# Kernel optimization log

Measured on AMD Instinct MI355X. Metric: run time of the kernel, lower is better.

Reference implementation:

```python
import jax, jax.numpy as jnp
import numpy as np

N = 100000
E = 1600000
D = 128          # f_gru_in == f_gru_out
G = 128          # f_gather
K = 4            # n_etypes
STEPS = 3        # n_gconv_steps


def setup_inputs() -> dict:
    key = jax.random.key(0)
    ks = jax.random.split(key, 16)
    s = 0.05
    return {
        "features": jax.random.normal(ks[0], (N, D), jnp.float32),
        "src": jax.random.randint(ks[1], (E,), 0, N, jnp.int32),
        "dst": jax.random.randint(ks[2], (E,), 0, N, jnp.int32),
        "etypes": jax.random.randint(ks[3], (E,), 0, K, jnp.int32),
        # per-etype edge linears (torch Linear: y = x W^T + b)
        "W_et": jax.random.normal(ks[4], (K, D, D), jnp.float32) * s,
        "b_et": jax.random.normal(ks[5], (K, D), jnp.float32) * s,
        # GRUCell weights, torch gate order (r, z, n)
        "W_ih": jax.random.normal(ks[6], (3 * D, D), jnp.float32) * s,
        "b_ih": jax.random.normal(ks[7], (3 * D,), jnp.float32) * s,
        "W_hh": jax.random.normal(ks[8], (3 * D, D), jnp.float32) * s,
        "b_hh": jax.random.normal(ks[9], (3 * D,), jnp.float32) * s,
        # gated output head
        "i_w": jax.random.normal(ks[10], (G, D + D), jnp.float32) * s,
        "i_b": jax.random.normal(ks[11], (G,), jnp.float32) * s,
        "j_w": jax.random.normal(ks[12], (G, D), jnp.float32) * s,
        "j_b": jax.random.normal(ks[13], (G,), jnp.float32) * s,
    }


def _gru_cell(a, h, W_ih, b_ih, W_hh, b_hh):
    gi = a @ W_ih.T + b_ih          # [N, 3D]
    gh = h @ W_hh.T + b_hh          # [N, 3D]
    ir, iz, in_ = jnp.split(gi, 3, axis=1)
    hr, hz, hn = jnp.split(gh, 3, axis=1)
    r = jax.nn.sigmoid(ir + hr)
    z = jax.nn.sigmoid(iz + hz)
    n = jnp.tanh(in_ + r * hn)
    return (1.0 - z) * n + z * h


def reference(features, src, dst, etypes, W_et, b_et, W_ih, b_ih, W_hh, b_hh,
              i_w, i_b, j_w, j_b):
    n_nodes = features.shape[0]
    h = features  # in_feats == out_feats -> no zero padding needed
    for _ in range(STEPS):
        # transform all nodes by every etype linear: [K, N, D]
        t = jnp.einsum('nd,kod->kno', h, W_et) + b_et[:, None, :]
        # gather per-edge message by (etype, src) then scatter-add to dst
        msg = t[etypes, src]                                  # [E, D]
        a = jax.ops.segment_sum(msg, dst, num_segments=n_nodes)
        h = _gru_cell(a, h, W_ih, b_ih, W_hh, b_hh)
    # dropout p=0 (eval) -> identity; gated output head
    gate = jax.nn.sigmoid(jnp.concatenate([h, features], axis=1) @ i_w.T + i_b)
    return gate * (h @ j_w.T + j_b)
```

## Files before the change

### kernel.cpp

```cpp
#include <hip/hip_runtime.h>
#include <hip/hip_bf16.h>

typedef __bf16 bf16;
typedef __attribute__((ext_vector_type(8))) __bf16 bf16x8;
typedef __attribute__((ext_vector_type(4))) float f32x4;

union BP { unsigned u; bf16 b[2]; };

struct Desc {
  const void* A1; const bf16* W1; int lda1;
  const void* A2; const bf16* W2; int lda2;
  const bf16* b1; const bf16* b2;
  int coff; int a2mode;
};
struct Desc4 { Desc d[4]; };

template<int NK>
__global__ __launch_bounds__(256) void gemm_k(Desc4 P, bf16* __restrict__ C, int ldc,
                                              int M, const int* __restrict__ flagp)
{
  const Desc d = P.d[blockIdx.y];
  const int lane = threadIdx.x & 63;
  const int w    = threadIdx.x >> 6;
  const int quad = lane >> 4;
  const int lr   = lane & 15;
  const int mbase = blockIdx.x * 128 + w * 32;

  __shared__ bf16 lds[128 * 136];

  f32x4 acc[2][8];
#pragma unroll
  for (int i = 0; i < 2; ++i)
#pragma unroll
    for (int j = 0; j < 8; ++j) acc[i][j] = (f32x4){0.f, 0.f, 0.f, 0.f};

  long r0 = mbase + lr;      if (r0 >= M) r0 = M - 1;
  long r1 = mbase + 16 + lr; if (r1 >= M) r1 = M - 1;

  {
    const bf16* A = (const bf16*)d.A1;
    const int lda = d.lda1;
#pragma unroll
    for (int kk = 0; kk < NK; ++kk) {
      const int kc = kk * 32 + quad * 8;
      bf16x8 a0 = *(const bf16x8*)(A + r0 * lda + kc);
      bf16x8 a1 = *(const bf16x8*)(A + r1 * lda + kc);
#pragma unroll
      for (int ct = 0; ct < 8; ++ct) {
        bf16x8 b = *(const bf16x8*)(d.W1 + ((size_t)(kk * 8 + ct) * 64 + lane) * 8);
        acc[0][ct] = __builtin_amdgcn_mfma_f32_16x16x32_bf16(a0, b, acc[0][ct], 0, 0, 0);
        acc[1][ct] = __builtin_amdgcn_mfma_f32_16x16x32_bf16(a1, b, acc[1][ct], 0, 0, 0);
      }
    }
  }
  if (d.a2mode != 0) {
    const int lda = d.lda2;
    const bool f32 = (d.a2mode == 2) && (*flagp != 0);
    if (f32) {
      const float* A = (const float*)d.A2;
#pragma unroll
      for (int kk = 0; kk < NK; ++kk) {
        const int kc = kk * 32 + quad * 8;
        f32x4 x0 = *(const f32x4*)(A + r0 * lda + kc);
        f32x4 x1 = *(const f32x4*)(A + r0 * lda + kc + 4);
        f32x4 y0 = *(const f32x4*)(A + r1 * lda + kc);
        f32x4 y1 = *(const f32x4*)(A + r1 * lda + kc + 4);
        bf16x8 a0, a1;
#pragma unroll
        for (int i = 0; i < 4; ++i) {
          a0[i] = (bf16)x0[i]; a0[i + 4] = (bf16)x1[i];
          a1[i] = (bf16)y0[i]; a1[i + 4] = (bf16)y1[i];
        }
#pragma unroll
        for (int ct = 0; ct < 8; ++ct) {
          bf16x8 b = *(const bf16x8*)(d.W2 + ((size_t)(kk * 8 + ct) * 64 + lane) * 8);
          acc[0][ct] = __builtin_amdgcn_mfma_f32_16x16x32_bf16(a0, b, acc[0][ct], 0, 0, 0);
          acc[1][ct] = __builtin_amdgcn_mfma_f32_16x16x32_bf16(a1, b, acc[1][ct], 0, 0, 0);
        }
      }
    } else {
      const bf16* A = (const bf16*)d.A2;
#pragma unroll
      for (int kk = 0; kk < NK; ++kk) {
        const int kc = kk * 32 + quad * 8;
        bf16x8 a0 = *(const bf16x8*)(A + r0 * lda + kc);
        bf16x8 a1 = *(const bf16x8*)(A + r1 * lda + kc);
#pragma unroll
        for (int ct = 0; ct < 8; ++ct) {
          bf16x8 b = *(const bf16x8*)(d.W2 + ((size_t)(kk * 8 + ct) * 64 + lane) * 8);
          acc[0][ct] = __builtin_amdgcn_mfma_f32_16x16x32_bf16(a0, b, acc[0][ct], 0, 0, 0);
          acc[1][ct] = __builtin_amdgcn_mfma_f32_16x16x32_bf16(a1, b, acc[1][ct], 0, 0, 0);
        }
      }
    }
  }

#pragma unroll
  for (int ct = 0; ct < 8; ++ct) {
    const int nl = ct * 16 + lr;
    float bv = 0.f;
    if (d.b1) bv += (float)d.b1[nl];
    if (d.b2) bv += (float)d.b2[nl];
#pragma unroll
    for (int rt = 0; rt < 2; ++rt) {
      const int rowb = w * 32 + rt * 16 + quad * 4;
#pragma unroll
      for (int r = 0; r < 4; ++r)
        lds[(rowb + r) * 136 + nl] = (bf16)(acc[rt][ct][r] + bv);
    }
  }
  __syncthreads();
  const int tr = threadIdx.x >> 4;
  const int tc = (threadIdx.x & 15) * 8;
#pragma unroll
  for (int i = 0; i < 8; ++i) {
    const int row = i * 16 + tr;
    const int grow = blockIdx.x * 128 + row;
    if (grow < M) {
      bf16x8 v = *(const bf16x8*)(lds + row * 136 + tc);
      *(bf16x8*)(C + (size_t)grow * ldc + d.coff + tc) = v;
    }
  }
}

__global__ __launch_bounds__(256) void fused_k(const bf16* __restrict__ big,
                                               bf16* __restrict__ hbp,
                                               const bf16* __restrict__ wb,
                                               int M)
{
  const int lane = threadIdx.x & 63;
  const int w    = threadIdx.x >> 6;
  const int quad = lane >> 4;
  const int lr   = lane & 15;
  const int mbase = blockIdx.x * 128 + w * 32;

  __shared__ bf16 lds[128 * 136];

  const bf16* wcat = wb;
  const bf16* blk  = wb + 69632;
  const bf16 *ih0 = blk,             *ih1 = blk + 16384, *ihn = blk + 2 * 16384;
  const bf16 *hh0 = blk + 3 * 16384, *hh1 = blk + 4 * 16384, *hhn = blk + 5 * 16384;
  const bf16 *bih = wb + 217088, *bhh = wb + 217472;

  long r0 = mbase + lr;      if (r0 >= M) r0 = M - 1;
  long r1 = mbase + 16 + lr; if (r1 >= M) r1 = M - 1;

  f32x4 acc[2][8];
#pragma unroll
  for (int i = 0; i < 2; ++i)
#pragma unroll
    for (int j = 0; j < 8; ++j) acc[i][j] = (f32x4){0.f, 0.f, 0.f, 0.f};

  bf16x8 Bb[2][8];
  bf16x8 Ab[4][2];
#pragma unroll
  for (int q = 0; q < 4; ++q) {
    const int kc = q * 32 + quad * 8;
    Ab[q][0] = *(const bf16x8*)(big + r0 * 544 + kc);
    Ab[q][1] = *(const bf16x8*)(big + r1 * 544 + kc);
  }
#pragma unroll
  for (int q = 0; q < 2; ++q) {
#pragma unroll
    for (int ct = 0; ct < 8; ++ct)
      Bb[q][ct] = *(const bf16x8*)(wcat + ((size_t)(q * 8 + ct) * 64 + lane) * 8);
  }
#pragma unroll
  for (int kk = 0; kk < 17; ++kk) {
    const int pa = kk & 3;
    const int pb = kk & 1;
#pragma unroll
    for (int ct = 0; ct < 8; ++ct) {
      acc[0][ct] = __builtin_amdgcn_mfma_f32_16x16x32_bf16(Ab[pa][0], Bb[pb][ct], acc[0][ct], 0, 0, 0);
      acc[1][ct] = __builtin_amdgcn_mfma_f32_16x16x32_bf16(Ab[pa][1], Bb[pb][ct], acc[1][ct], 0, 0, 0);
    }
    if (kk + 4 < 17) {
      const int k4 = kk + 4;
      const int kc = k4 * 32 + quad * 8;
      Ab[pa][0] = *(const bf16x8*)(big + r0 * 544 + kc);
      Ab[pa][1] = *(const bf16x8*)(big + r1 * 544 + kc);
    }
    if (kk + 2 < 17) {
      const int k2 = kk + 2;
#pragma unroll
      for (int ct = 0; ct < 8; ++ct)
        Bb[pb][ct] = *(const bf16x8*)(wcat + ((size_t)(k2 * 8 + ct) * 64 + lane) * 8);
    }
  }

  bf16x8 hf[2][4];
#pragma unroll
  for (int kk = 0; kk < 4; ++kk) {
    hf[0][kk] = *(const bf16x8*)(hbp + r0 * 128 + kk * 32 + quad * 8);
    hf[1][kk] = *(const bf16x8*)(hbp + r1 * 128 + kk * 32 + quad * 8);
  }

#pragma unroll
  for (int ct = 0; ct < 8; ++ct) {
    const int nl = ct * 16 + lr;
#pragma unroll
    for (int rt = 0; rt < 2; ++rt) {
      const int rowb = w * 32 + rt * 16 + quad * 4;
#pragma unroll
      for (int r = 0; r < 4; ++r)
        lds[(rowb + r) * 136 + nl] = (bf16)acc[rt][ct][r];
    }
  }
  bf16x8 af[2][4];
#pragma unroll
  for (int kk = 0; kk < 4; ++kk) {
    af[0][kk] = *(const bf16x8*)(lds + (w * 32 + lr) * 136 + kk * 32 + quad * 8);
    af[1][kk] = *(const bf16x8*)(lds + (w * 32 + 16 + lr) * 136 + kk * 32 + quad * 8);
  }
#pragma unroll
  for (int kk = 0; kk < 4; ++kk) {
    *(bf16x8*)(lds + (w * 32 + lr) * 136 + kk * 32 + quad * 8)      = hf[0][kk];
    *(bf16x8*)(lds + (w * 32 + 16 + lr) * 136 + kk * 32 + quad * 8) = hf[1][kk];
  }

  bf16x8 Gb[2][6];
#pragma unroll
  for (int q = 0; q < 2; ++q) {
    const size_t wi = ((size_t)(q * 8 + 0) * 64 + lane) * 8;
    Gb[q][0] = *(const bf16x8*)(ih0 + wi);
    Gb[q][1] = *(const bf16x8*)(hh0 + wi);
    Gb[q][2] = *(const bf16x8*)(ih1 + wi);
    Gb[q][3] = *(const bf16x8*)(hh1 + wi);
    Gb[q][4] = *(const bf16x8*)(ihn + wi);
    Gb[q][5] = *(const bf16x8*)(hhn + wi);
  }

#pragma unroll
  for (int ch = 0; ch < 8; ++ch) {
    f32x4 c[4][2];
#pragma unroll
    for (int s = 0; s < 4; ++s)
#pragma unroll
      for (int i = 0; i < 2; ++i) c[s][i] = (f32x4){0.f, 0.f, 0.f, 0.f};

#pragma unroll
    for (int kk = 0; kk < 4; ++kk) {
      const int G = ch * 4 + kk;
      const int p = G & 1;
      c[0][0] = __builtin_amdgcn_mfma_f32_16x16x32_bf16(af[0][kk], Gb[p][0], c[0][0], 0, 0, 0);
      c[0][1] = __builtin_amdgcn_mfma_f32_16x16x32_bf16(af[1][kk], Gb[p][0], c[0][1], 0, 0, 0);
      c[0][0] = __builtin_amdgcn_mfma_f32_16x16x32_bf16(hf[0][kk], Gb[p][1], c[0][0], 0, 0, 0);
      c[0][1] = __builtin_amdgcn_mfma_f32_16x16x32_bf16(hf[1][kk], Gb[p][1], c[0][1], 0, 0, 0);
      c[1][0] = __builtin_amdgcn_mfma_f32_16x16x32_bf16(af[0][kk], Gb[p][2], c[1][0], 0, 0, 0);
      c[1][1] = __builtin_amdgcn_mfma_f32_16x16x32_bf16(af[1][kk], Gb[p][2], c[1][1], 0, 0, 0);
      c[1][0] = __builtin_amdgcn_mfma_f32_16x16x32_bf16(hf[0][kk], Gb[p][3], c[1][0], 0, 0, 0);
      c[1][1] = __builtin_amdgcn_mfma_f32_16x16x32_bf16(hf[1][kk], Gb[p][3], c[1][1], 0, 0, 0);
      c[2][0] = __builtin_amdgcn_mfma_f32_16x16x32_bf16(af[0][kk], Gb[p][4], c[2][0], 0, 0, 0);
      c[2][1] = __builtin_amdgcn_mfma_f32_16x16x32_bf16(af[1][kk], Gb[p][4], c[2][1], 0, 0, 0);
      c[3][0] = __builtin_amdgcn_mfma_f32_16x16x32_bf16(hf[0][kk], Gb[p][5], c[3][0], 0, 0, 0);
      c[3][1] = __builtin_amdgcn_mfma_f32_16x16x32_bf16(hf[1][kk], Gb[p][5], c[3][1], 0, 0, 0);
      if (G + 2 < 32) {
        const int G2 = G + 2;
        const int ch2 = G2 >> 2, kk2 = G2 & 3;
        const int ct2 = ch2;
        const size_t wi2 = ((size_t)(kk2 * 8 + ct2) * 64 + lane) * 8;
        Gb[p][0] = *(const bf16x8*)(ih0 + wi2);
        Gb[p][1] = *(const bf16x8*)(hh0 + wi2);
        Gb[p][2] = *(const bf16x8*)(ih1 + wi2);
        Gb[p][3] = *(const bf16x8*)(hh1 + wi2);
        Gb[p][4] = *(const bf16x8*)(ihn + wi2);
        Gb[p][5] = *(const bf16x8*)(hhn + wi2);
      }
    }
    {
      const int col = ch * 16 + lr;
      const float br = (float)bih[col]       + (float)bhh[col];
      const float bz = (float)bih[128 + col] + (float)bhh[128 + col];
      const float bi = (float)bih[256 + col];
      const float bh = (float)bhh[256 + col];
#pragma unroll
      for (int rt = 0; rt < 2; ++rt) {
        const int rowb = w * 32 + rt * 16 + quad * 4;
#pragma unroll
        for (int r = 0; r < 4; ++r) {
          const int li = (rowb + r) * 136 + col;
          const float hv = (float)lds[li];
          const float rr = 1.f / (1.f + __expf(-(c[0][rt][r] + br)));
          const float zz = 1.f / (1.f + __expf(-(c[1][rt][r] + bz)));
          const float xn = c[2][rt][r] + bi + rr * (c[3][rt][r] + bh);
          const float e2 = __expf(2.f * xn);
          const float nn = 1.f - 2.f / (e2 + 1.f);
          lds[li] = (bf16)((1.f - zz) * nn + zz * hv);
        }
      }
    }
  }

  __syncthreads();
  const int tr = threadIdx.x >> 4;
  const int tc = (threadIdx.x & 15) * 8;
#pragma unroll
  for (int i = 0; i < 8; ++i) {
    const int row = i * 16 + tr;
    const int grow = blockIdx.x * 128 + row;
    if (grow < M) {
      bf16x8 v = *(const bf16x8*)(lds + row * 136 + tc);
      *(bf16x8*)(hbp + (size_t)grow * 128 + tc) = v;
    }
  }
}

__global__ __launch_bounds__(256) void detect_k(const unsigned short* __restrict__ f,
                                                int n16, int* __restrict__ flag)
{
  int i = blockIdx.x * 256 + threadIdx.x;
  int bad = 0;
  for (int j = i; j < n16; j += 256 * 1024) {
    int ex = (f[j] >> 7) & 0xFF;
    if (ex >= 0x87) bad = 1;
  }
  if (bad) atomicAdd(flag, 1);
}

__global__ __launch_bounds__(256) void feat_k(const void* __restrict__ src,
                                              bf16* __restrict__ hb, int n,
                                              const int* __restrict__ flag)
{
  int i = blockIdx.x * 256 + threadIdx.x;
  if (i >= n) return;
  if (*flag) hb[i] = (bf16)((const float*)src)[i];
  else       hb[i] = ((const bf16*)src)[i];
}

__global__ __launch_bounds__(256) void cvtw_k(
    const void* w_et, const void* b_et, const void* w_ih, const void* b_ih,
    const void* w_hh, const void* b_hh, const void* i_w, const void* i_b,
    const void* j_w, const void* j_b, bf16* __restrict__ wb,
    const int* __restrict__ flagp)
{
  int i = blockIdx.x * 256 + threadIdx.x;
  if (i >= 218112) return;
  const bool f32 = (*flagp != 0);
  auto rd = [&](const void* p, int idx) -> float {
    return f32 ? ((const float*)p)[idx] : (float)((const bf16*)p)[idx];
  };
  float v;
  if (i < 69632) {
    int e = i, j = e & 7, lane = (e >> 3) & 63, ct = (e >> 9) & 7, kk = e >> 12;
    int n = ct * 16 + (lane & 15), k = kk * 32 + (lane >> 4) * 8 + j;
    if (k < 512)      v = rd(w_et, (k >> 7) * 16384 + n * 128 + (k & 127));
    else if (k < 516) v = rd(b_et, (k - 512) * 128 + n);
    else              v = 0.f;
  } else if (i < 217088) {
    int blk = (i - 69632) >> 14, e = (i - 69632) & 16383;
    int j = e & 7, lane = (e >> 3) & 63, ct = (e >> 9) & 7, kk = e >> 12;
    int n = ct * 16 + (lane & 15), k = kk * 32 + (lane >> 4) * 8 + j;
    const void* src; int idx;
    switch (blk) {
      case 0: src = w_ih; idx = n * 128 + k; break;
      case 1: src = w_ih; idx = (128 + n) * 128 + k; break;
      case 2: src = w_ih; idx = (256 + n) * 128 + k; break;
      case 3: src = w_hh; idx = n * 128 + k; break;
      case 4: src = w_hh; idx = (128 + n) * 128 + k; break;
      case 5: src = w_hh; idx = (256 + n) * 128 + k; break;
      case 6: src = i_w;  idx = n * 256 + k; break;
      case 7: src = i_w;  idx = n * 256 + 128 + k; break;
      default: src = j_w; idx = n * 128 + k; break;
    }
    v = rd(src, idx);
  } else {
    int o = i - 217088;
    if (o < 384)      v = rd(b_ih, o);
    else if (o < 768) v = rd(b_hh, o - 384);
    else if (o < 896) v = rd(i_b, o - 768);
    else              v = rd(j_b, o - 896);
  }
  wb[i] = (bf16)v;
}

__global__ __launch_bounds__(256) void hist_k(const int* __restrict__ dst,
                                              const int* __restrict__ ety,
                                              int* __restrict__ deg, int E)
{
  int e = blockIdx.x * 256 + threadIdx.x;
  if (e < E) atomicAdd(&deg[dst[e] * 4 + ety[e]], 1);
}

__global__ __launch_bounds__(512) void scan1_k(const int* __restrict__ deg, int* __restrict__ rp,
                                               int* __restrict__ part, int n)
{
  __shared__ int buf[512];
  int i = blockIdx.x * 512 + threadIdx.x;
  int v = (i < n) ? deg[i] : 0;
  buf[threadIdx.x] = v;
  __syncthreads();
#pragma unroll
  for (int off = 1; off < 512; off <<= 1) {
    int t = 0;
    if (threadIdx.x >= off) t = buf[threadIdx.x - off];
    __syncthreads();
    buf[threadIdx.x] += t;
    __syncthreads();
  }
  if (i < n) rp[i] = buf[threadIdx.x] - v;
  if (threadIdx.x == 511) part[blockIdx.x] = buf[511];
}

__global__ __launch_bounds__(1024) void scan2_k(int* __restrict__ part, int nb, int* __restrict__ total)
{
  __shared__ int buf[1024];
  int t0 = threadIdx.x;
  int v = (t0 < nb) ? part[t0] : 0;
  buf[t0] = v;
  __syncthreads();
#pragma unroll
  for (int off = 1; off < 1024; off <<= 1) {
    int t = 0;
    if (t0 >= off) t = buf[t0 - off];
    __syncthreads();
    buf[t0] += t;
    __syncthreads();
  }
  if (t0 < nb) part[t0] = buf[t0] - v;
  if (t0 == 1023) *total = buf[1023];
}

__global__ __launch_bounds__(512) void scan3_k(int* __restrict__ rp, const int* __restrict__ part, int n)
{
  int i = blockIdx.x * 512 + threadIdx.x;
  if (i < n) rp[i] += part[blockIdx.x];
}

__global__ __launch_bounds__(256) void fill_k(const int* __restrict__ src, const int* __restrict__ dst,
                                              const int* __restrict__ ety, const int* __restrict__ rp,
                                              int* __restrict__ fil, int* __restrict__ bkt, int E)
{
  int e = blockIdx.x * 256 + threadIdx.x;
  if (e < E) {
    int key = dst[e] * 4 + ety[e];
    int pos = rp[key] + atomicAdd(&fil[key], 1);
    bkt[pos] = src[e];
  }
}

__global__ __launch_bounds__(256) void agg_k(const bf16* __restrict__ hb,
                                             const int* __restrict__ rp,
                                             const int* __restrict__ bkt,
                                             bf16* __restrict__ aggH, int N)
{
  const int lane = threadIdx.x & 63;
  const int n = blockIdx.x * 4 + (threadIdx.x >> 6);
  if (n >= N) return;
  const unsigned* hp = (const unsigned*)hb;
  unsigned* outp = (unsigned*)aggH + (size_t)n * 272;
  const int e0 = rp[n * 4];
  const int e1 = rp[n * 4 + 1];
  const int e2 = rp[n * 4 + 2];
  const int e3 = rp[n * 4 + 3];
  const int e4 = rp[n * 4 + 4];
  const int last = e4 - 1;
  float a00 = 0.f, a01 = 0.f, a10 = 0.f, a11 = 0.f;
  float a20 = 0.f, a21 = 0.f, a30 = 0.f, a31 = 0.f;
  for (int base = e0; base < e4; base += 8) {
    int b[8];
#pragma unroll
    for (int t = 0; t < 8; ++t) {
      const int i = base + t;
      b[t] = bkt[i <= last ? i : last];
    }
    unsigned u[8];
#pragma unroll
    for (int t = 0; t < 8; ++t)
      u[t] = hp[(size_t)b[t] * 64 + lane];
#pragma unroll
    for (int t = 0; t < 8; ++t) {
      const int i = base + t;
      BP tt; tt.u = u[t];
      const bool ok = (i <= last);
      const float v0 = ok ? (float)tt.b[0] : 0.f;
      const float v1 = ok ? (float)tt.b[1] : 0.f;
      const bool s0 = i < e1;
      const bool s1 = (i >= e1) && (i < e2);
      const bool s2 = (i >= e2) && (i < e3);
      const bool s3 = (i >= e3);
      a00 += s0 ? v0 : 0.f;  a01 += s0 ? v1 : 0.f;
      a10 += s1 ? v0 : 0.f;  a11 += s1 ? v1 : 0.f;
      a20 += s2 ? v0 : 0.f;  a21 += s2 ? v1 : 0.f;
      a30 += s3 ? v0 : 0.f;  a31 += s3 ? v1 : 0.f;
    }
  }
  BP o;
  o.b[0] = (bf16)a00; o.b[1] = (bf16)a01; outp[0 * 64 + lane] = o.u;
  o.b[0] = (bf16)a10; o.b[1] = (bf16)a11; outp[1 * 64 + lane] = o.u;
  o.b[0] = (bf16)a20; o.b[1] = (bf16)a21; outp[2 * 64 + lane] = o.u;
  o.b[0] = (bf16)a30; o.b[1] = (bf16)a31; outp[3 * 64 + lane] = o.u;
  if (lane < 16) {
    BP z; z.b[0] = (bf16)0.f; z.b[1] = (bf16)0.f;
    if (lane == 0) { z.b[0] = (bf16)(float)(e1 - e0); z.b[1] = (bf16)(float)(e2 - e1); }
    if (lane == 1) { z.b[0] = (bf16)(float)(e3 - e2); z.b[1] = (bf16)(float)(e4 - e3); }
    outp[256 + lane] = z.u;
  }
}

__global__ __launch_bounds__(256) void head_k(const bf16* __restrict__ G,
                                              void* __restrict__ out, int N,
                                              const int* __restrict__ flag)
{
  int i = blockIdx.x * 256 + threadIdx.x;
  if (i >= N * 64) return;
  int n = i >> 6, l = i & 63;
  const unsigned* g = (const unsigned*)G + (size_t)n * 128;
  BP gl, uu;
  gl.u = g[l]; uu.u = g[64 + l];
  float v0 = (float)uu.b[0] / (1.f + expf(-(float)gl.b[0]));
  float v1 = (float)uu.b[1] / (1.f + expf(-(float)gl.b[1]));
  if (*flag) {
    ((float*)out)[(size_t)n * 128 + 2 * l]     = v0;
    ((float*)out)[(size_t)n * 128 + 2 * l + 1] = v1;
  } else {
    BP o; o.b[0] = (bf16)v0; o.b[1] = (bf16)v1;
    ((unsigned*)out)[(size_t)n * 64 + l] = o.u;
  }
}

extern "C" void kernel_launch(void* const* d_in, const int* in_sizes, int n_in,
                              void* d_out, int out_size, void* d_ws, size_t ws_size,
                              hipStream_t stream)
{
  const void* feat = d_in[0];
  const int*  src  = (const int*)d_in[1];
  const int*  dst  = (const int*)d_in[2];
  const int*  ety  = (const int*)d_in[3];

  const int N = in_sizes[0] / 128;
  const int E = in_sizes[1];
  const int total = N * 128;

  char* p = (char*)d_ws;
  auto alloc = [&](size_t bytes) -> char* {
    char* q = p;
    p += (bytes + 255) & ~(size_t)255;
    return q;
  };
  bf16* big  = (bf16*)alloc((size_t)N * 544 * 2);
  bf16* hb   = (bf16*)alloc((size_t)total * 2);
  bf16* wb   = (bf16*)alloc(218112 * 2);
  int*  rp   = (int*) alloc(((size_t)4 * N + 1) * 4);
  int*  deg  = (int*) alloc((size_t)4 * N * 4);
  int*  bkt  = (int*) alloc((size_t)E * 4);
  int*  part = (int*) alloc(1024 * 4);
  int*  flag = (int*) alloc(64);

  const int oBlk = 69632;
  const bf16 *iwa = wb + oBlk + 6 * 16384, *iwb = wb + oBlk + 7 * 16384,
             *jw  = wb + oBlk + 8 * 16384;
  const bf16 *ib = wb + 217856, *jb = wb + 217984;

  const int gE  = (E + 255) / 256;
  const int gT  = (total + 255) / 256;
  const int gM  = (N + 127) / 128;
  const int n4  = 4 * N;
  const int gS  = (n4 + 511) / 512;
  const int gH  = (N * 64 + 255) / 256;

  hipMemsetAsync(flag, 0, 4, stream);
  detect_k<<<1024, 256, 0, stream>>>((const unsigned short*)feat, 2000000, flag);
  feat_k<<<gT, 256, 0, stream>>>(feat, hb, total, flag);
  cvtw_k<<<(218112 + 255) / 256, 256, 0, stream>>>(
      d_in[4], d_in[5], d_in[6], d_in[7], d_in[8],
      d_in[9], d_in[10], d_in[11], d_in[12], d_in[13], wb, flag);

  hipMemsetAsync(deg, 0, (size_t)n4 * 4, stream);
  hist_k<<<gE, 256, 0, stream>>>(dst, ety, deg, E);
  scan1_k<<<gS, 512, 0, stream>>>(deg, rp, part, n4);
  scan2_k<<<1, 1024, 0, stream>>>(part, gS, rp + n4);
  scan3_k<<<gS, 512, 0, stream>>>(rp, part, n4);
  hipMemsetAsync(deg, 0, (size_t)n4 * 4, stream);
  fill_k<<<gE, 256, 0, stream>>>(src, dst, ety, rp, deg, bkt, E);

  Desc4 Ph = {};
  Ph.d[0] = { hb, iwa, 128, feat, iwb, 128, ib, nullptr, 0,   2 };
  Ph.d[1] = { hb, jw,  128, nullptr, nullptr, 0, jb, nullptr, 128, 0 };

  for (int step = 0; step < 3; ++step) {
    agg_k<<<(N + 3) / 4, 256, 0, stream>>>(hb, rp, bkt, big, N);
    fused_k<<<gM, 256, 0, stream>>>(big, hb, wb, N);
  }

  gemm_k<4><<<dim3(gM, 2), 256, 0, stream>>>(Ph, big, 256, N, flag);
  head_k<<<gH, 256, 0, stream>>>(big, d_out, N, flag);
}
```

Measured before the change: 996.1 us.

## Stage fused-kernel weight tiles through LDS via async global_load_lds double buffering

In the fused GRU kernel, each wave used to load weight fragments straight from global memory into registers, so all four waves fetched the same weights. Now each block loads every weight tile into a double-buffered LDS region once, using global_load_lds DMA, and waves read their fragments from LDS. The aim is to cut redundant global/L2 traffic and register pressure, which could allow more waves per CU. In exchange it adds a __syncthreads per k-step (17 in the first GEMM, 32 in the gate loop), turns the outer gate loop into a non-unrolled loop, and adds 16KB of LDS per block, which may lower occupancy.

```diff
diff --git a/kernel.cpp b/kernel.cpp
--- a/kernel.cpp
+++ b/kernel.cpp
@@ -6,6 +6,12 @@
 typedef __attribute__((ext_vector_type(4))) float f32x4;
 
 union BP { unsigned u; bf16 b[2]; };
+
+__device__ __forceinline__ void dma16(const void* g, void* l) {
+  __builtin_amdgcn_global_load_lds(
+      (const __attribute__((address_space(1))) unsigned*)g,
+      (__attribute__((address_space(3))) unsigned*)l, 16, 0, 0);
+}
 
 struct Desc {
   const void* A1; const bf16* W1; int lda1;
@@ -26,7 +32,7 @@
   const int lr   = lane & 15;
   const int mbase = blockIdx.x * 128 + w * 32;
 
-  __shared__ bf16 lds[128 * 136];
+  __shared__ __align__(16) bf16 lds[128 * 136];
 
   f32x4 acc[2][8];
 #pragma unroll
@@ -134,7 +140,8 @@
   const int lr   = lane & 15;
   const int mbase = blockIdx.x * 128 + w * 32;
 
-  __shared__ bf16 lds[128 * 136];
+  __shared__ __align__(16) bf16 lds[128 * 136];
+  __shared__ __align__(16) bf16 wlds[2][4096];
 
   const bf16* wcat = wb;
   const bf16* blk  = wb + 69632;
@@ -145,47 +152,50 @@
   long r0 = mbase + lr;      if (r0 >= M) r0 = M - 1;
   long r1 = mbase + 16 + lr; if (r1 >= M) r1 = M - 1;
 
+  dma16(wcat + (size_t)(w * 2)     * 512 + (size_t)lane * 8, &wlds[0][(w * 2) * 512]);
+  dma16(wcat + (size_t)(w * 2 + 1) * 512 + (size_t)lane * 8, &wlds[0][(w * 2 + 1) * 512]);
+  bf16x8 Ab[2][2];
+  Ab[0][0] = *(const bf16x8*)(big + r0 * 544 + quad * 8);
+  Ab[0][1] = *(const bf16x8*)(big + r1 * 544 + quad * 8);
+
   f32x4 acc[2][8];
 #pragma unroll
   for (int i = 0; i < 2; ++i)
 #pragma unroll
     for (int j = 0; j < 8; ++j) acc[i][j] = (f32x4){0.f, 0.f, 0.f, 0.f};
 
-  bf16x8 Bb[2][8];
-  bf16x8 Ab[4][2];
-#pragma unroll
-  for (int q = 0; q < 4; ++q) {
-    const int kc = q * 32 + quad * 8;
-    Ab[q][0] = *(const bf16x8*)(big + r0 * 544 + kc);
-    Ab[q][1] = *(const bf16x8*)(big + r1 * 544 + kc);
-  }
-#pragma unroll
-  for (int q = 0; q < 2; ++q) {
-#pragma unroll
-    for (int ct = 0; ct < 8; ++ct)
-      Bb[q][ct] = *(const bf16x8*)(wcat + ((size_t)(q * 8 + ct) * 64 + lane) * 8);
-  }
+  __syncthreads();
+
 #pragma unroll
   for (int kk = 0; kk < 17; ++kk) {
-    const int pa = kk & 3;
-    const int pb = kk & 1;
+    const int cur = kk & 1;
+    const int nxt = cur ^ 1;
+    if (kk + 1 < 17) {
+      const size_t gb = (size_t)(kk + 1) * 4096;
+      dma16(wcat + gb + (size_t)(w * 2)     * 512 + (size_t)lane * 8, &wlds[nxt][(w * 2) * 512]);
+      dma16(wcat + gb + (size_t)(w * 2 + 1) * 512 + (size_t)lane * 8, &wlds[nxt][(w * 2 + 1) * 512]);
+      const int kc = (kk + 1) * 32 + quad * 8;
+      Ab[nxt][0] = *(const bf16x8*)(big + r0 * 544 + kc);
+      Ab[nxt][1] = *(const bf16x8*)(big + r1 * 544 + kc);
+    }
 #pragma unroll
     for (int ct = 0; ct < 8; ++ct) {
-      acc[0][ct] = __builtin_amdgcn_mfma_f32_16x16x32_bf16(Ab[pa][0], Bb[pb][ct], acc[0][ct], 0, 0, 0);
-      acc[1][ct] = __builtin_amdgcn_mfma_f32_16x16x32_bf16(Ab[pa][1], Bb[pb][ct], acc[1][ct], 0, 0, 0);
-    }
-    if (kk + 4 < 17) {
-      const int k4 = kk + 4;
-      const int kc = k4 * 32 + quad * 8;
-      Ab[pa][0] = *(const bf16x8*)(big + r0 * 544 + kc);
-      Ab[pa][1] = *(const bf16x8*)(big + r1 * 544 + kc);
-    }
-    if (kk + 2 < 17) {
-      const int k2 = kk + 2;
-#pragma unroll
-      for (int ct = 0; ct < 8; ++ct)
-        Bb[pb][ct] = *(const bf16x8*)(wcat + ((size_t)(k2 * 8 + ct) * 64 + lane) * 8);
-    }
+      bf16x8 b = *(const bf16x8*)&wlds[cur][(ct * 64 + lane) * 8];
+      acc[0][ct] = __builtin_amdgcn_mfma_f32_16x16x32_bf16(Ab[cur][0], b, acc[0][ct], 0, 0, 0);
+      acc[1][ct] = __builtin_amdgcn_mfma_f32_16x16x32_bf16(Ab[cur][1], b, acc[1][ct], 0, 0, 0);
+    }
+    __syncthreads();
+  }
+
+  const bf16* wptr0 = ih0; const bf16* wptr1 = hh0; const bf16* wptr2 = ih1;
+  const bf16* wptr3 = hh1; const bf16* wptr4 = ihn; const bf16* wptr5 = hhn;
+  {
+    if (w == 0) { dma16(wptr0 + (size_t)lane * 8, &wlds[0][0 * 512]);
+                  dma16(wptr4 + (size_t)lane * 8, &wlds[0][4 * 512]); }
+    if (w == 1) { dma16(wptr1 + (size_t)lane * 8, &wlds[0][1 * 512]);
+                  dma16(wptr5 + (size_t)lane * 8, &wlds[0][5 * 512]); }
+    if (w == 2) { dma16(wptr2 + (size_t)lane * 8, &wlds[0][2 * 512]); }
+    if (w == 3) { dma16(wptr3 + (size_t)lane * 8, &wlds[0][3 * 512]); }
   }
 
   bf16x8 hf[2][4];
@@ -194,7 +204,6 @@
     hf[0][kk] = *(const bf16x8*)(hbp + r0 * 128 + kk * 32 + quad * 8);
     hf[1][kk] = *(const bf16x8*)(hbp + r1 * 128 + kk * 32 + quad * 8);
   }
-
 #pragma unroll
   for (int ct = 0; ct < 8; ++ct) {
     const int nl = ct * 16 + lr;
@@ -217,20 +226,9 @@
     *(bf16x8*)(lds + (w * 32 + lr) * 136 + kk * 32 + quad * 8)      = hf[0][kk];
     *(bf16x8*)(lds + (w * 32 + 16 + lr) * 136 + kk * 32 + quad * 8) = hf[1][kk];
   }
-
-  bf16x8 Gb[2][6];
-#pragma unroll
-  for (int q = 0; q < 2; ++q) {
-    const size_t wi = ((size_t)(q * 8 + 0) * 64 + lane) * 8;
-    Gb[q][0] = *(const bf16x8*)(ih0 + wi);
-    Gb[q][1] = *(const bf16x8*)(hh0 + wi);
-    Gb[q][2] = *(const bf16x8*)(ih1 + wi);
-    Gb[q][3] = *(const bf16x8*)(hh1 + wi);
-    Gb[q][4] = *(const bf16x8*)(ihn + wi);
-    Gb[q][5] = *(const bf16x8*)(hhn + wi);
-  }
-
-#pragma unroll
+  __syncthreads();
+
+#pragma unroll 1
   for (int ch = 0; ch < 8; ++ch) {
     f32x4 c[4][2];
 #pragma unroll
@@ -240,58 +238,64 @@
 
 #pragma unroll
     for (int kk = 0; kk < 4; ++kk) {
-      const int G = ch * 4 + kk;
-      const int p = G & 1;
-      c[0][0] = __builtin_amdgcn_mfma_f32_16x16x32_bf16(af[0][kk], Gb[p][0], c[0][0], 0, 0, 0);
-      c[0][1] = __builtin_amdgcn_mfma_f32_16x16x32_bf16(af[1][kk], Gb[p][0], c[0][1], 0, 0, 0);
-      c[0][0] = __builtin_amdgcn_mfma_f32_16x16x32_bf16(hf[0][kk], Gb[p][1], c[0][0], 0, 0, 0);
-      c[0][1] = __builtin_amdgcn_mfma_f32_16x16x32_bf16(hf[1][kk], Gb[p][1], c[0][1], 0, 0, 0);
-      c[1][0] = __builtin_amdgcn_mfma_f32_16x16x32_bf16(af[0][kk], Gb[p][2], c[1][0], 0, 0, 0);
-      c[1][1] = __builtin_amdgcn_mfma_f32_16x16x32_bf16(af[1][kk], Gb[p][2], c[1][1], 0, 0, 0);
-      c[1][0] = __builtin_amdgcn_mfma_f32_16x16x32_bf16(hf[0][kk], Gb[p][3], c[1][0], 0, 0, 0);
-      c[1][1] = __builtin_amdgcn_mfma_f32_16x16x32_bf16(hf[1][kk], Gb[p][3], c[1][1], 0, 0, 0);
-      c[2][0] = __builtin_amdgcn_mfma_f32_16x16x32_bf16(af[0][kk], Gb[p][4], c[2][0], 0, 0, 0);
-      c[2][1] = __builtin_amdgcn_mfma_f32_16x16x32_bf16(af[1][kk], Gb[p][4], c[2][1], 0, 0, 0);
-      c[3][0] = __builtin_amdgcn_mfma_f32_16x16x32_bf16(hf[0][kk], Gb[p][5], c[3][0], 0, 0, 0);
-      c[3][1] = __builtin_amdgcn_mfma_f32_16x16x32_bf16(hf[1][kk], Gb[p][5], c[3][1], 0, 0, 0);
-      if (G + 2 < 32) {
-        const int G2 = G + 2;
-        const int ch2 = G2 >> 2, kk2 = G2 & 3;
-        const int ct2 = ch2;
-        const size_t wi2 = ((size_t)(kk2 * 8 + ct2) * 64 + lane) * 8;
-        Gb[p][0] = *(const bf16x8*)(ih0 + wi2);
-        Gb[p][1] = *(const bf16x8*)(hh0 + wi2);
-        Gb[p][2] = *(const bf16x8*)(ih1 + wi2);
-        Gb[p][3] = *(const bf16x8*)(hh1 + wi2);
-        Gb[p][4] = *(const bf16x8*)(ihn + wi2);
-        Gb[p][5] = *(const bf16x8*)(hhn + wi2);
+      const int cur = kk & 1;
+      const int nx  = cur ^ 1;
+      {
+        size_t koff;
+        if (kk < 3) koff = (size_t)((kk + 1) * 8 + ch) * 512;
+        else        koff = (size_t)(ch < 7 ? ch + 1 : 7) * 512;
+        if (w == 0) { dma16(wptr0 + koff + (size_t)lane * 8, &wlds[nx][0 * 512]);
+                      dma16(wptr4 + koff + (size_t)lane * 8, &wlds[nx][4 * 512]); }
+        if (w == 1) { dma16(wptr1 + koff + (size_t)lane * 8, &wlds[nx][1 * 512]);
+                      dma16(wptr5 + koff + (size_t)lane * 8, &wlds[nx][5 * 512]); }
+        if (w == 2) { dma16(wptr2 + koff + (size_t)lane * 8, &wlds[nx][2 * 512]); }
+        if (w == 3) { dma16(wptr3 + koff + (size_t)lane * 8, &wlds[nx][3 * 512]); }
       }
-    }
-    {
-      const int col = ch * 16 + lr;
-      const float br = (float)bih[col]       + (float)bhh[col];
-      const float bz = (float)bih[128 + col] + (float)bhh[128 + col];
-      const float bi = (float)bih[256 + col];
-      const float bh = (float)bhh[256 + col];
-#pragma unroll
-      for (int rt = 0; rt < 2; ++rt) {
-        const int rowb = w * 32 + rt * 16 + quad * 4;
-#pragma unroll
-        for (int r = 0; r < 4; ++r) {
-          const int li = (rowb + r) * 136 + col;
-          const float hv = (float)lds[li];
-          const float rr = 1.f / (1.f + __expf(-(c[0][rt][r] + br)));
-          const float zz = 1.f / (1.f + __expf(-(c[1][rt][r] + bz)));
-          const float xn = c[2][rt][r] + bi + rr * (c[3][rt][r] + bh);
-          const float e2 = __expf(2.f * xn);
-          const float nn = 1.f - 2.f / (e2 + 1.f);
-          lds[li] = (bf16)((1.f - zz) * nn + zz * hv);
+      bf16x8 g0 = *(const bf16x8*)&wlds[cur][(0 * 64 + lane) * 8];
+      bf16x8 g1 = *(const bf16x8*)&wlds[cur][(1 * 64 + lane) * 8];
+      bf16x8 g2 = *(const bf16x8*)&wlds[cur][(2 * 64 + lane) * 8];
+      bf16x8 g3 = *(const bf16x8*)&wlds[cur][(3 * 64 + lane) * 8];
+      bf16x8 g4 = *(const bf16x8*)&wlds[cur][(4 * 64 + lane) * 8];
+      bf16x8 g5 = *(const bf16x8*)&wlds[cur][(5 * 64 + lane) * 8];
+      c[0][0] = __builtin_amdgcn_mfma_f32_16x16x32_bf16(af[0][kk], g0, c[0][0], 0, 0, 0);
+      c[0][1] = __builtin_amdgcn_mfma_f32_16x16x32_bf16(af[1][kk], g0, c[0][1], 0, 0, 0);
+      c[0][0] = __builtin_amdgcn_mfma_f32_16x16x32_bf16(hf[0][kk], g1, c[0][0], 0, 0, 0);
+      c[0][1] = __builtin_amdgcn_mfma_f32_16x16x32_bf16(hf[1][kk], g1, c[0][1], 0, 0, 0);
+      c[1][0] = __builtin_amdgcn_mfma_f32_16x16x32_bf16(af[0][kk], g2, c[1][0], 0, 0, 0);
+      c[1][1] = __builtin_amdgcn_mfma_f32_16x16x32_bf16(af[1][kk], g2, c[1][1], 0, 0, 0);
+      c[1][0] = __builtin_amdgcn_mfma_f32_16x16x32_bf16(hf[0][kk], g3, c[1][0], 0, 0, 0);
+      c[1][1] = __builtin_amdgcn_mfma_f32_16x16x32_bf16(hf[1][kk], g3, c[1][1], 0, 0, 0);
+      c[2][0] = __builtin_amdgcn_mfma_f32_16x16x32_bf16(af[0][kk], g4, c[2][0], 0, 0, 0);
+      c[2][1] = __builtin_amdgcn_mfma_f32_16x16x32_bf16(af[1][kk], g4, c[2][1], 0, 0, 0);
+      c[3][0] = __builtin_amdgcn_mfma_f32_16x16x32_bf16(hf[0][kk], g5, c[3][0], 0, 0, 0);
+      c[3][1] = __builtin_amdgcn_mfma_f32_16x16x32_bf16(hf[1][kk], g5, c[3][1], 0, 0, 0);
+
+      if (kk == 3) {
+        const int col = ch * 16 + lr;
+        const float br = (float)bih[col]       + (float)bhh[col];
+        const float bz = (float)bih[128 + col] + (float)bhh[128 + col];
+        const float bi = (float)bih[256 + col];
+        const float bh = (float)bhh[256 + col];
+#pragma unroll
+        for (int rt = 0; rt < 2; ++rt) {
+          const int rowb = w * 32 + rt * 16 + quad * 4;
+#pragma unroll
+          for (int r = 0; r < 4; ++r) {
+            const int li = (rowb + r) * 136 + col;
+            const float hv = (float)lds[li];
+            const float rr = 1.f / (1.f + __expf(-(c[0][rt][r] + br)));
+            const float zz = 1.f / (1.f + __expf(-(c[1][rt][r] + bz)));
+            const float xn = c[2][rt][r] + bi + rr * (c[3][rt][r] + bh);
+            const float e2 = __expf(2.f * xn);
+            const float nn = 1.f - 2.f / (e2 + 1.f);
+            lds[li] = (bf16)((1.f - zz) * nn + zz * hv);
+          }
         }
       }
-    }
-  }
-
-  __syncthreads();
+      __syncthreads();
+    }
+  }
+
   const int tr = threadIdx.x >> 4;
   const int tc = (threadIdx.x & 15) * 8;
 #pragma unroll
```

Measured after the change: 948.4 us. -4.8%, faster.
